# Optimization experiments

Measured on AMD Instinct MI355X. Metric: run time of the kernel, lower is better.

The kernel has to match this reference:

```python
import jax, jax.numpy as jnp
import numpy as np

D = 256   # feature_dim
NQ = 512  # num query keypoints
NK = 512  # num key/value keypoints


def setup_inputs() -> dict:
    key = jax.random.key(0)
    ks = jax.random.split(key, 10)
    def w(k, shape, fan_in):
        return jax.random.normal(k, shape, dtype=jnp.float32) / np.sqrt(fan_in)
    inp = {
        "x": jax.random.normal(ks[0], (1, D, NQ), dtype=jnp.float32),
        "source": jax.random.normal(ks[1], (1, D, NK), dtype=jnp.float32),
        # MLPAttention score MLP: Conv1d(2D->D,k=1), ReLU, Conv1d(D->1,k=1)
        "w1": w(ks[2], (D, 2 * D), 2 * D),
        "b1": w(ks[3], (D,), 2 * D),
        "w2": w(ks[4], (1, D), D),
        "b2": w(ks[5], (1,), D),
        # outer MLP: Conv1d(2D->2D,k=1), ReLU, Conv1d(2D->D,k=1) with zero bias init
        "wa": w(ks[6], (2 * D, 2 * D), 2 * D),
        "ba": w(ks[7], (2 * D,), 2 * D),
        "wb": w(ks[8], (D, 2 * D), 2 * D),
        "bb": jnp.zeros((D,), dtype=jnp.float32),
    }
    return inp


def reference(x, source, w1, b1, w2, b2, wa, ba, wb, bb):
    d = x.shape[1]
    q = x[0]       # [D, nq]
    k = source[0]  # [D, nk]
    # cat((q broadcast over nk, k broadcast over nq)) then Conv1d(2D->D) is
    # equivalent to splitting w1 into query/key halves and broadcasting:
    w1q, w1k = w1[:, :d], w1[:, d:]
    aq = w1q @ q + b1[:, None]                       # [D, nq]
    ak = w1k @ k                                     # [D, nk]
    h = jax.nn.relu(aq[:, :, None] + ak[:, None, :])  # [D, nq, nk]
    scores = (jnp.einsum('d,dnm->nm', w2[0], h) + b2[0])[None]  # [1, nq, nk]
    prob = jax.nn.softmax(scores, axis=-1)
    message = jnp.einsum('bnm,bdm->bdn', prob, source)  # [1, D, nq]
    # outer MLP on cat([x, message], channel dim)
    cat = jnp.concatenate([x, message], axis=1)         # [1, 2D, nq]
    h2 = jax.nn.relu(jnp.einsum('oc,bcn->bon', wa, cat) + ba[None, :, None])
    y = jnp.einsum('oc,bcn->bon', wb, h2) + bb[None, :, None]  # [1, D, nq]
    return (y, scores)
```

## Files before the change

kernel.cpp:

```cpp
#include <hip/hip_runtime.h>
#include <hip/hip_bf16.h>

#define DD 256
#define NN 512

typedef __attribute__((ext_vector_type(8))) short short8;
typedef __attribute__((ext_vector_type(4))) float floatx4;

__device__ __forceinline__ unsigned short f2bf(float f) {
  unsigned u = __float_as_uint(f);
  u += 0x7FFFu + ((u >> 16) & 1u);
  return (unsigned short)(u >> 16);
}
__device__ __forceinline__ unsigned pack2(float a, float b) {
  return (unsigned)f2bf(a) | ((unsigned)f2bf(b) << 16);
}

__device__ __forceinline__ short8 ldfrag(const unsigned short* __restrict__ base,
                                         int row, int ld, int k, int lane) {
  return *(const short8*)(base + (row + (lane & 15)) * ld + k + ((lane >> 4) << 3));
}

__device__ __forceinline__ short8 ldfrag_f32(const float* __restrict__ base,
                                             int row, int ld, int k, int lane) {
  const float* p = base + (row + (lane & 15)) * ld + k + ((lane >> 4) << 3);
  const float4 v0 = *(const float4*)p;
  const float4 v1 = *(const float4*)(p + 4);
  short8 r;
  r[0] = (short)f2bf(v0.x); r[1] = (short)f2bf(v0.y);
  r[2] = (short)f2bf(v0.z); r[3] = (short)f2bf(v0.w);
  r[4] = (short)f2bf(v1.x); r[5] = (short)f2bf(v1.y);
  r[6] = (short)f2bf(v1.z); r[7] = (short)f2bf(v1.w);
  return r;
}

__device__ __forceinline__ short8 ldfragT_g(const float* __restrict__ base,
                                            int n0, int ld, int k, int lane) {
  const int n = n0 + (lane & 15);
  const int kk = k + ((lane >> 4) << 3);
  short8 r;
#pragma unroll
  for (int j = 0; j < 8; ++j) r[j] = (short)f2bf(base[(kk + j) * ld + n]);
  return r;
}

template <int NF>
__device__ __forceinline__ void acc_zero(floatx4 acc[NF]) {
#pragma unroll
  for (int i = 0; i < NF; ++i) {
    acc[i][0] = 0.f; acc[i][1] = 0.f; acc[i][2] = 0.f; acc[i][3] = 0.f;
  }
}

template <int NF>
__device__ __forceinline__ void ksplit_combine(floatx4 acc[NF], float* red,
                                               int wave, int lane) {
  const int W = 16 * NF;
  const int col = lane & 15;
  const int q = lane >> 4;
  if (wave > 0) {
    float* base = red + (wave - 1) * 16 * W;
#pragma unroll
    for (int nf = 0; nf < NF; ++nf)
#pragma unroll
      for (int r = 0; r < 4; ++r)
        base[(q * 4 + r) * W + nf * 16 + col] = acc[nf][r];
  }
  __syncthreads();
  if (wave == 0) {
#pragma unroll
    for (int nf = 0; nf < NF; ++nf)
#pragma unroll
      for (int r = 0; r < 4; ++r) {
        const int idx = (q * 4 + r) * W + nf * 16 + col;
        acc[nf][r] += red[idx] + red[16 * W + idx] + red[32 * W + idx];
      }
  }
}

template <int NF, bool COLBIAS, bool ROWBIAS, bool RELU, bool OUTBF>
__device__ __forceinline__ void gemm_epi(floatx4 acc[NF],
    const float* __restrict__ bias, void* __restrict__ C, int ldc,
    int m0, int n0, int lane) {
  const int col = lane & 15;
  const int q = lane >> 4;
#pragma unroll
  for (int nf = 0; nf < NF; ++nf) {
    const int n = n0 + nf * 16 + col;
    const float cb = COLBIAS ? bias[n] : 0.0f;
#pragma unroll
    for (int r = 0; r < 4; ++r) {
      const int m = m0 + q * 4 + r;
      float v = acc[nf][r] + cb + (ROWBIAS ? bias[m] : 0.0f);
      if (RELU) v = fmaxf(v, 0.0f);
      if (OUTBF) ((unsigned short*)C)[m * ldc + n] = f2bf(v);
      else       ((float*)C)[m * ldc + n] = v;
    }
  }
}

__global__ __launch_bounds__(256) void aqak_kernel(
    const float* __restrict__ x, const float* __restrict__ src,
    const float* __restrict__ w1, const float* __restrict__ b1,
    const float* __restrict__ bb,
    float* __restrict__ aq, float* __restrict__ ak, float* __restrict__ y) {
  __shared__ float red[1536];

  const int tid = threadIdx.x;
  const int z = blockIdx.z;

  if (z == 2) {
    const int o = blockIdx.y * 16 + blockIdx.x;
    const float bv = bb[o];
    float2 v; v.x = bv; v.y = bv;
    *(float2*)&y[o * NN + tid * 2] = v;
    return;
  }

  const int lane = tid & 63;
  const int wave = tid >> 6;
  const int m0 = blockIdx.y * 16;
  const int n0 = blockIdx.x * 32;
  const float* in = z ? src : x;

  floatx4 acc[2]; acc_zero<2>(acc);
#pragma unroll
  for (int kc = 0; kc < 2; ++kc) {
    const int kl = wave * 64 + kc * 32;
    short8 a = ldfrag_f32(w1, m0, NN, z * 256 + kl, lane);
#pragma unroll
    for (int nf = 0; nf < 2; ++nf) {
      short8 b = ldfragT_g(in, n0 + nf * 16, NN, kl, lane);
      acc[nf] = __builtin_amdgcn_mfma_f32_16x16x32_bf16(a, b, acc[nf], 0, 0, 0);
    }
  }
  ksplit_combine<2>(acc, red, wave, lane);
  if (wave == 0) {
    if (z == 0) gemm_epi<2, false, true, false, false>(acc, b1, aq, NN, m0, n0, lane);
    else        gemm_epi<2, false, false, false, false>(acc, nullptr, ak, NN, m0, n0, lane);
  }
}

__global__ __launch_bounds__(256) void scores_kernel(
    const float* __restrict__ aq, const float* __restrict__ ak,
    const float* __restrict__ w2, const float* __restrict__ b2,
    float* __restrict__ sc) {
  __shared__ float aqs[128][32];
  __shared__ float aks[128][32];
  __shared__ float w2s[DD];

  const int tid = threadIdx.x;
  const int n0 = blockIdx.x * 32;
  const int m0 = blockIdx.y * 32;
  const int tn = tid & 31;
  const int tm4 = (tid >> 5) * 4;

  w2s[tid] = w2[tid];

  float s0 = 0.f, s1 = 0.f, s2 = 0.f, s3 = 0.f;
  for (int d0 = 0; d0 < DD; d0 += 128) {
    __syncthreads();
#pragma unroll
    for (int k = 0; k < 16; ++k) {
      const int idx = k * 256 + tid;
      const int r = idx >> 5, cc = idx & 31;
      aqs[r][cc] = aq[(d0 + r) * NN + n0 + cc];
      aks[r][cc] = ak[(d0 + r) * NN + m0 + cc];
    }
    __syncthreads();
    for (int dd = 0; dd < 128; ++dd) {
      const float w = w2s[d0 + dd];
      const float a = aqs[dd][tn];
      const float4 akv = *(const float4*)&aks[dd][tm4];
      s0 += w * fmaxf(a + akv.x, 0.f);
      s1 += w * fmaxf(a + akv.y, 0.f);
      s2 += w * fmaxf(a + akv.z, 0.f);
      s3 += w * fmaxf(a + akv.w, 0.f);
    }
  }
  const float bv = b2[0];
  float4 o; o.x = s0 + bv; o.y = s1 + bv; o.z = s2 + bv; o.w = s3 + bv;
  *(float4*)&sc[(n0 + tn) * NN + m0 + tm4] = o;
}

__global__ __launch_bounds__(256) void msgT_kernel(
    const float* __restrict__ sc, const float* __restrict__ srcf,
    unsigned short* __restrict__ msgTb) {
  __shared__ unsigned short Ap[16][520];
  __shared__ float red[1536];
  __shared__ float smax[16][16];
  __shared__ float ssum[16][16];
  __shared__ float rst[16][2];

  const int tid = threadIdx.x;
  const int lane = tid & 63;
  const int wave = tid >> 6;
  const int n0 = blockIdx.y * 16;
  const int d0 = blockIdx.x * 32;

  const int r = tid >> 4;
  const int c = tid & 15;
  float4 v[8];
  const float* rp = sc + (n0 + r) * NN + c * 4;
#pragma unroll
  for (int i = 0; i < 8; ++i) v[i] = *(const float4*)(rp + i * 64);

  float mx = -3.0e38f;
#pragma unroll
  for (int i = 0; i < 8; ++i)
    mx = fmaxf(mx, fmaxf(fmaxf(v[i].x, v[i].y), fmaxf(v[i].z, v[i].w)));
  smax[r][c] = mx;
  __syncthreads();
  if (c == 0) {
    float m2 = smax[r][0];
#pragma unroll
    for (int i = 1; i < 16; ++i) m2 = fmaxf(m2, smax[r][i]);
    rst[r][0] = m2;
  }
  __syncthreads();
  mx = rst[r][0];

  float sum = 0.f;
#pragma unroll
  for (int i = 0; i < 8; ++i) {
    v[i].x = __expf(v[i].x - mx); v[i].y = __expf(v[i].y - mx);
    v[i].z = __expf(v[i].z - mx); v[i].w = __expf(v[i].w - mx);
    sum += v[i].x + v[i].y + v[i].z + v[i].w;
  }
  ssum[r][c] = sum;
  __syncthreads();
  if (c == 0) {
    float s2 = ssum[r][0];
#pragma unroll
    for (int i = 1; i < 16; ++i) s2 += ssum[r][i];
    rst[r][1] = s2;
  }
  __syncthreads();
  const float inv = 1.0f / rst[r][1];
#pragma unroll
  for (int i = 0; i < 8; ++i) {
    *(unsigned*)&Ap[r][c * 4 + i * 64]     = pack2(v[i].x * inv, v[i].y * inv);
    *(unsigned*)&Ap[r][c * 4 + i * 64 + 2] = pack2(v[i].z * inv, v[i].w * inv);
  }
  __syncthreads();

  floatx4 acc[2]; acc_zero<2>(acc);
  const int k0w = wave * 128;
  const int arow = lane & 15;
  const int koff = (lane >> 4) << 3;
#pragma unroll
  for (int k = 0; k < 128; k += 32) {
    short8 a = *(const short8*)&Ap[arow][k0w + k + koff];
#pragma unroll
    for (int nf = 0; nf < 2; ++nf) {
      short8 b = ldfrag_f32(srcf, d0 + nf * 16, NN, k0w + k, lane);
      acc[nf] = __builtin_amdgcn_mfma_f32_16x16x32_bf16(a, b, acc[nf], 0, 0, 0);
    }
  }
  ksplit_combine<2>(acc, red, wave, lane);
  if (wave == 0)
    gemm_epi<2, false, false, false, true>(acc, nullptr, msgTb, DD, n0, d0, lane);
}

__global__ __launch_bounds__(256) void h2y_kernel(
    const float* __restrict__ x, const unsigned short* __restrict__ msgTb,
    const float* __restrict__ waf, const float* __restrict__ wbf,
    const float* __restrict__ ba, float* __restrict__ y) {
  __shared__ __align__(16) unsigned short h2L[16][72];

  const int tid = threadIdx.x;
  const int lane = tid & 63;
  const int wave = tid >> 6;
  const int o0 = blockIdx.x * 64;
  const int n0g = blockIdx.y * 16;

  {
    floatx4 acc;
    acc[0] = 0.f; acc[1] = 0.f; acc[2] = 0.f; acc[3] = 0.f;
    const int ow = o0 + wave * 16;
#pragma unroll
    for (int kc = 0; kc < 16; ++kc) {
      const int c0 = kc * 32;
      short8 a = (c0 < 256) ? ldfragT_g(x, n0g, NN, c0, lane)
                            : ldfrag(msgTb, n0g, DD, c0 - 256, lane);
      short8 b = ldfrag_f32(waf, ow, NN, c0, lane);
      acc = __builtin_amdgcn_mfma_f32_16x16x32_bf16(a, b, acc, 0, 0, 0);
    }
    const int col = lane & 15, q = lane >> 4;
    const float cb = ba[o0 + wave * 16 + col];
#pragma unroll
    for (int r = 0; r < 4; ++r)
      h2L[q * 4 + r][wave * 16 + col] = f2bf(fmaxf(acc[r] + cb, 0.f));
  }
  __syncthreads();

  {
    const int brow = lane & 15;
    const int koff = (lane >> 4) << 3;
    const int col = lane & 15, q = lane >> 4;
#pragma unroll
    for (int t = 0; t < 4; ++t) {
      const int o2t = wave * 64 + t * 16;
      floatx4 acc;
      acc[0] = 0.f; acc[1] = 0.f; acc[2] = 0.f; acc[3] = 0.f;
#pragma unroll
      for (int kc = 0; kc < 2; ++kc) {
        short8 a = ldfrag_f32(wbf, o2t, NN, o0 + kc * 32, lane);
        short8 b = *(const short8*)&h2L[brow][kc * 32 + koff];
        acc = __builtin_amdgcn_mfma_f32_16x16x32_bf16(a, b, acc, 0, 0, 0);
      }
#pragma unroll
      for (int r = 0; r < 4; ++r)
        atomicAdd(&y[(o2t + q * 4 + r) * NN + n0g + col], acc[r]);
    }
  }
}

extern "C" void kernel_launch(void* const* d_in, const int* in_sizes, int n_in,
                              void* d_out, int out_size, void* d_ws, size_t ws_size,
                              hipStream_t stream) {
  (void)in_sizes; (void)n_in; (void)out_size; (void)ws_size;

  const float* x   = (const float*)d_in[0];
  const float* src = (const float*)d_in[1];
  const float* w1  = (const float*)d_in[2];
  const float* b1  = (const float*)d_in[3];
  const float* w2  = (const float*)d_in[4];
  const float* b2  = (const float*)d_in[5];
  const float* wa  = (const float*)d_in[6];
  const float* ba  = (const float*)d_in[7];
  const float* wb  = (const float*)d_in[8];
  const float* bb  = (const float*)d_in[9];

  float* y_out  = (float*)d_out;
  float* sc_out = (float*)d_out + 131072;

  char* ws = (char*)d_ws;
  float*          aq    = (float*)(ws);
  float*          ak    = (float*)(ws + (512 << 10));
  unsigned short* msgTb = (unsigned short*)(ws + (1024 << 10));

  aqak_kernel<<<dim3(16, 16, 3), 256, 0, stream>>>(x, src, w1, b1, bb, aq, ak, y_out);
  scores_kernel<<<dim3(16, 16), 256, 0, stream>>>(aq, ak, w2, b2, sc_out);
  msgT_kernel<<<dim3(8, 32), 256, 0, stream>>>(sc_out, src, msgTb);
  h2y_kernel<<<dim3(8, 32), 256, 0, stream>>>(x, msgTb, wa, wb, ba, y_out);
}
```

Measured before the change: 105.0 us.

## Register-block scores kernel with split-D waves and pre-transpose x to bf16

```diff
diff --git a/kernel.cpp b/kernel.cpp
--- a/kernel.cpp
+++ b/kernel.cpp
@@ -103,17 +103,23 @@
     const float* __restrict__ x, const float* __restrict__ src,
     const float* __restrict__ w1, const float* __restrict__ b1,
     const float* __restrict__ bb,
-    float* __restrict__ aq, float* __restrict__ ak, float* __restrict__ y) {
+    float* __restrict__ aq, float* __restrict__ ak, float* __restrict__ y,
+    unsigned short* __restrict__ xT) {
   __shared__ float red[1536];
 
   const int tid = threadIdx.x;
   const int z = blockIdx.z;
 
   if (z == 2) {
-    const int o = blockIdx.y * 16 + blockIdx.x;
-    const float bv = bb[o];
+    const int c = blockIdx.y * 16 + blockIdx.x;
+    const float bv = bb[c];
     float2 v; v.x = bv; v.y = bv;
-    *(float2*)&y[o * NN + tid * 2] = v;
+    *(float2*)&y[c * NN + tid * 2] = v;
+    const int n0t = c * 2 + (tid >> 7);
+    const int d2 = (tid & 127) * 2;
+    const float f0 = x[d2 * NN + n0t];
+    const float f1 = x[(d2 + 1) * NN + n0t];
+    *(unsigned*)&xT[n0t * DD + d2] = pack2(f0, f1);
     return;
   }
 
@@ -145,42 +151,74 @@
     const float* __restrict__ aq, const float* __restrict__ ak,
     const float* __restrict__ w2, const float* __restrict__ b2,
     float* __restrict__ sc) {
-  __shared__ float aqs[128][32];
-  __shared__ float aks[128][32];
+  __shared__ __align__(16) float aqs[256][36];
+  __shared__ __align__(16) float aks[256][36];
+  __shared__ __align__(16) float part[4][32][32];
   __shared__ float w2s[DD];
 
   const int tid = threadIdx.x;
+  const int lane = tid & 63;
+  const int wave = tid >> 6;
   const int n0 = blockIdx.x * 32;
   const int m0 = blockIdx.y * 32;
-  const int tn = tid & 31;
-  const int tm4 = (tid >> 5) * 4;
 
   w2s[tid] = w2[tid];
 
-  float s0 = 0.f, s1 = 0.f, s2 = 0.f, s3 = 0.f;
-  for (int d0 = 0; d0 < DD; d0 += 128) {
-    __syncthreads();
-#pragma unroll
-    for (int k = 0; k < 16; ++k) {
-      const int idx = k * 256 + tid;
-      const int r = idx >> 5, cc = idx & 31;
-      aqs[r][cc] = aq[(d0 + r) * NN + n0 + cc];
-      aks[r][cc] = ak[(d0 + r) * NN + m0 + cc];
-    }
-    __syncthreads();
-    for (int dd = 0; dd < 128; ++dd) {
-      const float w = w2s[d0 + dd];
-      const float a = aqs[dd][tn];
-      const float4 akv = *(const float4*)&aks[dd][tm4];
-      s0 += w * fmaxf(a + akv.x, 0.f);
-      s1 += w * fmaxf(a + akv.y, 0.f);
-      s2 += w * fmaxf(a + akv.z, 0.f);
-      s3 += w * fmaxf(a + akv.w, 0.f);
-    }
-  }
-  const float bv = b2[0];
-  float4 o; o.x = s0 + bv; o.y = s1 + bv; o.z = s2 + bv; o.w = s3 + bv;
-  *(float4*)&sc[(n0 + tn) * NN + m0 + tm4] = o;
+#pragma unroll
+  for (int i = 0; i < 8; ++i) {
+    const int idx = i * 256 + tid;
+    const int row = idx >> 3;
+    const int c4 = (idx & 7) * 4;
+    *(float4*)&aqs[row][c4] = *(const float4*)&aq[row * NN + n0 + c4];
+    *(float4*)&aks[row][c4] = *(const float4*)&ak[row * NN + m0 + c4];
+  }
+  __syncthreads();
+
+  {
+    const int nq = lane & 7;
+    const int mq = lane >> 3;
+    float s[4][4];
+#pragma unroll
+    for (int i = 0; i < 4; ++i)
+#pragma unroll
+      for (int j = 0; j < 4; ++j) s[i][j] = 0.f;
+
+    const int dbeg = wave * 64;
+    for (int dd = dbeg; dd < dbeg + 64; ++dd) {
+      const float4 a4 = *(const float4*)&aqs[dd][nq * 4];
+      const float4 k4 = *(const float4*)&aks[dd][mq * 4];
+      const float w = w2s[dd];
+      const float a[4] = {a4.x, a4.y, a4.z, a4.w};
+      const float k[4] = {k4.x, k4.y, k4.z, k4.w};
+#pragma unroll
+      for (int i = 0; i < 4; ++i)
+#pragma unroll
+        for (int j = 0; j < 4; ++j)
+          s[i][j] += w * fmaxf(a[i] + k[j], 0.f);
+    }
+#pragma unroll
+    for (int i = 0; i < 4; ++i) {
+      float4 o; o.x = s[i][0]; o.y = s[i][1]; o.z = s[i][2]; o.w = s[i][3];
+      *(float4*)&part[wave][nq * 4 + i][mq * 4] = o;
+    }
+  }
+  __syncthreads();
+
+  {
+    const int n = tid >> 3;
+    const int mg = (tid & 7) * 4;
+    const float4 p0 = *(const float4*)&part[0][n][mg];
+    const float4 p1 = *(const float4*)&part[1][n][mg];
+    const float4 p2 = *(const float4*)&part[2][n][mg];
+    const float4 p3 = *(const float4*)&part[3][n][mg];
+    const float bv = b2[0];
+    float4 o;
+    o.x = p0.x + p1.x + p2.x + p3.x + bv;
+    o.y = p0.y + p1.y + p2.y + p3.y + bv;
+    o.z = p0.z + p1.z + p2.z + p3.z + bv;
+    o.w = p0.w + p1.w + p2.w + p3.w + bv;
+    *(float4*)&sc[(n0 + n) * NN + m0 + mg] = o;
+  }
 }
 
 __global__ __launch_bounds__(256) void msgT_kernel(
@@ -263,7 +301,7 @@
 }
 
 __global__ __launch_bounds__(256) void h2y_kernel(
-    const float* __restrict__ x, const unsigned short* __restrict__ msgTb,
+    const unsigned short* __restrict__ xT, const unsigned short* __restrict__ msgTb,
     const float* __restrict__ waf, const float* __restrict__ wbf,
     const float* __restrict__ ba, float* __restrict__ y) {
   __shared__ __align__(16) unsigned short h2L[16][72];
@@ -281,7 +319,7 @@
 #pragma unroll
     for (int kc = 0; kc < 16; ++kc) {
       const int c0 = kc * 32;
-      short8 a = (c0 < 256) ? ldfragT_g(x, n0g, NN, c0, lane)
+      short8 a = (c0 < 256) ? ldfrag(xT, n0g, DD, c0, lane)
                             : ldfrag(msgTb, n0g, DD, c0 - 256, lane);
       short8 b = ldfrag_f32(waf, ow, NN, c0, lane);
       acc = __builtin_amdgcn_mfma_f32_16x16x32_bf16(a, b, acc, 0, 0, 0);
@@ -339,9 +377,11 @@
   float*          aq    = (float*)(ws);
   float*          ak    = (float*)(ws + (512 << 10));
   unsigned short* msgTb = (unsigned short*)(ws + (1024 << 10));
-
-  aqak_kernel<<<dim3(16, 16, 3), 256, 0, stream>>>(x, src, w1, b1, bb, aq, ak, y_out);
+  unsigned short* xT    = (unsigned short*)(ws + (1280 << 10));
+
+  aqak_kernel<<<dim3(16, 16, 3), 256, 0, stream>>>(x, src, w1, b1, bb, aq, ak,
+                                                   y_out, xT);
   scores_kernel<<<dim3(16, 16), 256, 0, stream>>>(aq, ak, w2, b2, sc_out);
   msgT_kernel<<<dim3(8, 32), 256, 0, stream>>>(sc_out, src, msgTb);
-  h2y_kernel<<<dim3(8, 32), 256, 0, stream>>>(x, msgTb, wa, wb, ba, y_out);
-}
+  h2y_kernel<<<dim3(8, 32), 256, 0, stream>>>(xT, msgTb, wa, wb, ba, y_out);
+}
```

New measurement: 104.7 us. No clear change (-0.3%).
